# Kernel optimization log

Hardware: AMD Instinct MI355X
Metric: run time of the kernel (lower is better)

Reference implementation:

```python
import jax, jax.numpy as jnp
import numpy as np

N = 10000       # nodes
E = 320000      # edges
D = 256         # feature dim (out_channels)
L = 5           # num_layers


def setup_inputs() -> dict:
    key = jax.random.key(0)
    ks = jax.random.split(key, 8)
    x = jax.random.normal(ks[0], (N, D), dtype=jnp.float32)
    edge_index = jax.random.randint(ks[1], (2, E), 0, N, dtype=jnp.int64)
    edge_attr = jax.random.uniform(ks[2], (E,), dtype=jnp.float32)
    s = 1.0 / np.sqrt(D)
    # per-layer message transform weights [L, D, D]
    weight = jax.random.uniform(ks[3], (L, D, D), minval=-s, maxval=s, dtype=jnp.float32)
    # GRUCell parameters (torch layout: [3D, D] rows = r, z, n)
    w_ih = jax.random.uniform(ks[4], (3 * D, D), minval=-s, maxval=s, dtype=jnp.float32)
    w_hh = jax.random.uniform(ks[5], (3 * D, D), minval=-s, maxval=s, dtype=jnp.float32)
    b_ih = jax.random.uniform(ks[6], (3 * D,), minval=-s, maxval=s, dtype=jnp.float32)
    b_hh = jax.random.uniform(ks[7], (3 * D,), minval=-s, maxval=s, dtype=jnp.float32)
    return {"x": x, "edge_index": edge_index, "edge_attr": edge_attr,
            "weight": weight, "w_ih": w_ih, "w_hh": w_hh,
            "b_ih": b_ih, "b_hh": b_hh}


def _gru_cell(inp, h, w_ih, w_hh, b_ih, b_hh):
    # torch.nn.GRUCell math
    gi = inp @ w_ih.T + b_ih    # [N, 3D]
    gh = h @ w_hh.T + b_hh      # [N, 3D]
    i_r, i_z, i_n = jnp.split(gi, 3, axis=-1)
    h_r, h_z, h_n = jnp.split(gh, 3, axis=-1)
    r = jax.nn.sigmoid(i_r + h_r)
    z = jax.nn.sigmoid(i_z + h_z)
    n = jnp.tanh(i_n + r * h_n)
    return (1.0 - z) * n + z * h


def reference(x, edge_index, edge_attr, weight, w_ih, w_hh, b_ih, b_hh):
    src, dst = edge_index[0], edge_index[1]
    h = x
    for l in range(L):
        m = h @ weight[l]                                   # [N, D]
        msg = m[src] * edge_attr[:, None]                   # [E, D]
        agg = jax.ops.segment_sum(msg, dst, num_segments=N)  # [N, D]
        h = _gru_cell(agg, h, w_ih, w_hh, b_ih, b_hh)
    return h
```

## Files before the change

### kernel.cpp

```cpp
#include <hip/hip_runtime.h>
#include <hip/hip_bf16.h>

#define NN 10000
#define NPAD 10048
#define EE 320000
#define DD 256
#define LL 5

typedef __bf16 bf16x8 __attribute__((ext_vector_type(8)));
typedef __bf16 bf16x4 __attribute__((ext_vector_type(4)));
typedef float f32x4 __attribute__((ext_vector_type(4)));

__device__ __forceinline__ void gload_lds16(const void* g, void* l) {
    __builtin_amdgcn_global_load_lds(
        (const __attribute__((address_space(1))) void*)g,
        (__attribute__((address_space(3))) void*)l, 16, 0, 0);
}


__global__ void zero_deg_k(int* __restrict__ deg) {
    int i = blockIdx.x * blockDim.x + threadIdx.x;
    if (i < NN) deg[i] = 0;
}

__global__ void hist_k(const int* __restrict__ dst, int* __restrict__ deg) {
    int e = blockIdx.x * blockDim.x + threadIdx.x;
    if (e < EE) atomicAdd(&deg[dst[e]], 1);
}

__global__ void scan_k(const int* __restrict__ deg, int* __restrict__ row_start,
                       int* __restrict__ cursor) {
    __shared__ int sums[1024];
    const int CH = 10;
    int t = threadIdx.x;
    int base = t * CH;
    int loc[CH];
    int s = 0;
#pragma unroll
    for (int i = 0; i < CH; i++) {
        int v = (base + i < NN) ? deg[base + i] : 0;
        loc[i] = s;
        s += v;
    }
    sums[t] = s;
    __syncthreads();
    for (int off = 1; off < 1024; off <<= 1) {
        int v = (t >= off) ? sums[t - off] : 0;
        __syncthreads();
        sums[t] += v;
        __syncthreads();
    }
    int pre = (t == 0) ? 0 : sums[t - 1];
#pragma unroll
    for (int i = 0; i < CH; i++) {
        int idx = base + i;
        if (idx < NN) {
            int v = pre + loc[i];
            row_start[idx] = v;
            cursor[idx] = v;
        }
    }
    if (t == 1023) row_start[NN] = sums[1023];
}

__global__ void fill_k(const int* __restrict__ ei, const float* __restrict__ attr,
                       int* __restrict__ cursor, int* __restrict__ ssrc,
                       float* __restrict__ sattr) {
    int e = blockIdx.x * blockDim.x + threadIdx.x;
    if (e < EE) {
        int dv = ei[EE + e];
        int p = atomicAdd(&cursor[dv], 1);
        ssrc[p] = ei[e];
        sattr[p] = attr[e];
    }
}


__global__ void transpose_wb_k(const float* __restrict__ W, __bf16* __restrict__ Wt) {
    __shared__ float t[32][33];
    int l = blockIdx.z;
    int bx = blockIdx.x * 32;
    int by = blockIdx.y * 32;
    for (int i = threadIdx.y; i < 32; i += 8)
        t[i][threadIdx.x] = W[l * 65536 + (by + i) * DD + bx + threadIdx.x];
    __syncthreads();
    for (int i = threadIdx.y; i < 32; i += 8)
        Wt[l * 65536 + (bx + i) * DD + by + threadIdx.x] = (__bf16)t[threadIdx.x][i];
}

__global__ void conv_gruw_k(const float* __restrict__ w_ih, const float* __restrict__ w_hh,
                            __bf16* __restrict__ wihb, __bf16* __restrict__ whhb) {
    int i = blockIdx.x * blockDim.x + threadIdx.x;
    if (i < 768 * 256) {
        wihb[i] = (__bf16)w_ih[i];
        whhb[i] = (__bf16)w_hh[i];
    }
}

__global__ void conv_x_k(const float* __restrict__ x, float* __restrict__ hb,
                         __bf16* __restrict__ hbf) {
    int i = blockIdx.x * blockDim.x + threadIdx.x;
    if (i < NN * DD) {
        float v = x[i];
        hb[i] = v;
        hbf[i] = (__bf16)v;
    }
}

__global__ void pad_zero_k(__bf16* __restrict__ a, __bf16* __restrict__ b,
                           __bf16* __restrict__ c, __bf16* __restrict__ d) {
    int i = blockIdx.x * blockDim.x + threadIdx.x;
    if (i < (NPAD - NN) * DD) {
        a[NN * DD + i] = (__bf16)0.f;
        b[NN * DD + i] = (__bf16)0.f;
        c[NN * DD + i] = (__bf16)0.f;
        d[NN * DD + i] = (__bf16)0.f;
    }
}


__global__ __launch_bounds__(256, 2)
void gemm_m_k(const __bf16* __restrict__ hbf, const __bf16* __restrict__ wt,
              __bf16* __restrict__ mout) {
    __shared__ __bf16 sA[64][32];
    __shared__ __bf16 sB[64][32];
    int tid = threadIdx.x;
    int wave = tid >> 6, lane = tid & 63;
    int ln = lane & 15, quad = lane >> 4;
    int rowBlock = blockIdx.x * 64;
    int colBlock = blockIdx.y * 64;
    int rowHalf = (wave >> 1) * 32;
    int colHalf = (wave & 1) * 32;
    int r4 = lane >> 2;
    int kb = (lane & 3) * 8;

    f32x4 acc[2][2] = {};

    for (int k0 = 0; k0 < DD; k0 += 32) {
        __syncthreads();
#pragma unroll
        for (int ii = 0; ii < 2; ii++) {
            int rg = (wave & 1) * 2 + ii;
            const __bf16* src;
            __bf16* dst;
            if (wave < 2) {
                src = hbf + (size_t)(rowBlock + rg * 16 + r4) * DD + k0 + kb;
                dst = &sA[rg * 16][0];
            } else {
                src = wt + (size_t)(colBlock + rg * 16 + r4) * DD + k0 + kb;
                dst = &sB[rg * 16][0];
            }
            gload_lds16(src, dst);
        }
        __syncthreads();

        bf16x8 af[2], bf[2];
#pragma unroll
        for (int i = 0; i < 2; i++)
            af[i] = *(const bf16x8*)&sA[rowHalf + i * 16 + ln][quad * 8];
#pragma unroll
        for (int cc = 0; cc < 2; cc++)
            bf[cc] = *(const bf16x8*)&sB[colHalf + cc * 16 + ln][quad * 8];
#pragma unroll
        for (int nf = 0; nf < 2; nf++)
#pragma unroll
            for (int cc = 0; cc < 2; cc++)
                acc[nf][cc] = __builtin_amdgcn_mfma_f32_16x16x32_bf16(af[nf], bf[cc], acc[nf][cc], 0, 0, 0);
    }
#pragma unroll
    for (int nf = 0; nf < 2; nf++)
#pragma unroll
        for (int r = 0; r < 4; r++) {
            int n = rowBlock + rowHalf + nf * 16 + quad * 4 + r;
#pragma unroll
            for (int cc = 0; cc < 2; cc++) {
                int d = colBlock + colHalf + cc * 16 + ln;
                mout[(size_t)n * DD + d] = (__bf16)acc[nf][cc][r];
            }
        }
}


__global__ __launch_bounds__(256)
void aggregate_bf_k(const __bf16* __restrict__ m, const int* __restrict__ row_start,
                    const int* __restrict__ ssrc, const float* __restrict__ sattr,
                    __bf16* __restrict__ aggb) {
    __shared__ int sIdx[4][64];
    __shared__ float sAtt[4][64];
    int w = threadIdx.x >> 6, lane = threadIdx.x & 63;
    int n = blockIdx.x * 4 + w;
    int s0 = row_start[n], s1 = row_start[n + 1];
    int half = lane >> 5;
    int c8 = (lane & 31) * 8;

    float acc[8] = {0.f, 0.f, 0.f, 0.f, 0.f, 0.f, 0.f, 0.f};

    for (int base = s0; base < s1; base += 64) {
        int cnt = min(64, s1 - base);
        if (lane < cnt) {
            sIdx[w][lane] = ssrc[base + lane];
            sAtt[w][lane] = sattr[base + lane];
        }
        int t = 0;
        for (; t + 8 <= cnt; t += 8) {
#pragma unroll
            for (int u = 0; u < 4; u++) {
                int e = t + u * 2 + half;
                int s = sIdx[w][e];
                float ww = sAtt[w][e];
                bf16x8 v = *(const bf16x8*)(m + (size_t)s * DD + c8);
#pragma unroll
                for (int i = 0; i < 8; i++) acc[i] += (float)v[i] * ww;
            }
        }
        for (; t + 2 <= cnt; t += 2) {
            int e = t + half;
            int s = sIdx[w][e];
            float ww = sAtt[w][e];
            bf16x8 v = *(const bf16x8*)(m + (size_t)s * DD + c8);
#pragma unroll
            for (int i = 0; i < 8; i++) acc[i] += (float)v[i] * ww;
        }
        if (t < cnt && half == 0) {
            int s = sIdx[w][t];
            float ww = sAtt[w][t];
            bf16x8 v = *(const bf16x8*)(m + (size_t)s * DD + c8);
#pragma unroll
            for (int i = 0; i < 8; i++) acc[i] += (float)v[i] * ww;
        }
    }

#pragma unroll
    for (int i = 0; i < 8; i++) acc[i] += __shfl_xor(acc[i], 32, 64);

    if (half == 0) {
        bf16x8 o;
#pragma unroll
        for (int i = 0; i < 8; i++) o[i] = (__bf16)acc[i];
        *(bf16x8*)(aggb + (size_t)n * DD + c8) = o;
    }
}


__global__ __launch_bounds__(256, 2)
void gru_mfma_k(const __bf16* __restrict__ aggb, const __bf16* __restrict__ hbf,
                const float* __restrict__ hin,
                const __bf16* __restrict__ wih, const __bf16* __restrict__ whh,
                const float* __restrict__ b_ih, const float* __restrict__ b_hh,
                float* __restrict__ hout, __bf16* __restrict__ hbfout) {
    __shared__ __bf16 sA[2][64][32];
    __shared__ __bf16 sB[6][64][32];
    int tid = threadIdx.x;
    int wave = tid >> 6, lane = tid & 63;
    int ln = lane & 15, quad = lane >> 4;
    int nodeBlock = blockIdx.x * 64;
    int colBlock = blockIdx.y * 64;
    int nodeHalf = (wave >> 1) * 32;
    int colHalf = (wave & 1) * 32;
    int r4 = lane >> 2;
    int kb = (lane & 3) * 8;

    f32x4 acc[6][2][2] = {};

    for (int k0 = 0; k0 < DD; k0 += 32) {
        __syncthreads();
#pragma unroll
        for (int ii = 0; ii < 8; ii++) {
            int idx = wave * 8 + ii;
            const __bf16* src;
            __bf16* dst;
            if (idx < 8) {
                int s = idx >> 2;
                int rg = idx & 3;
                const __bf16* A = s ? hbf : aggb;
                src = A + (size_t)(nodeBlock + rg * 16 + r4) * DD + k0 + kb;
                dst = &sA[s][rg * 16][0];
            } else {
                int j = idx - 8;
                int g6 = j >> 2;
                int rg = j & 3;
                const __bf16* B = (g6 < 3) ? wih : whh;
                int brow = (g6 % 3) * 256 + colBlock + rg * 16 + r4;
                src = B + (size_t)brow * DD + k0 + kb;
                dst = &sB[g6][rg * 16][0];
            }
            gload_lds16(src, dst);
        }
        __syncthreads();

        bf16x8 aA[2], aH[2];
#pragma unroll
        for (int nf = 0; nf < 2; nf++) {
            aA[nf] = *(const bf16x8*)&sA[0][nodeHalf + nf * 16 + ln][quad * 8];
            aH[nf] = *(const bf16x8*)&sA[1][nodeHalf + nf * 16 + ln][quad * 8];
        }
#pragma unroll
        for (int g = 0; g < 3; g++) {
#pragma unroll
            for (int cc = 0; cc < 2; cc++) {
                bf16x8 bI = *(const bf16x8*)&sB[g][colHalf + cc * 16 + ln][quad * 8];
                bf16x8 bH = *(const bf16x8*)&sB[3 + g][colHalf + cc * 16 + ln][quad * 8];
#pragma unroll
                for (int nf = 0; nf < 2; nf++) {
                    acc[g][nf][cc] = __builtin_amdgcn_mfma_f32_16x16x32_bf16(aA[nf], bI, acc[g][nf][cc], 0, 0, 0);
                    acc[3 + g][nf][cc] = __builtin_amdgcn_mfma_f32_16x16x32_bf16(aH[nf], bH, acc[3 + g][nf][cc], 0, 0, 0);
                }
            }
        }
    }

#pragma unroll
    for (int nf = 0; nf < 2; nf++) {
#pragma unroll
        for (int r = 0; r < 4; r++) {
            int n = nodeBlock + nodeHalf + nf * 16 + quad * 4 + r;
            if (n >= NN) continue;
#pragma unroll
            for (int cc = 0; cc < 2; cc++) {
                int d = colBlock + colHalf + cc * 16 + ln;
                float ir = acc[0][nf][cc][r] + b_ih[d];
                float iz = acc[1][nf][cc][r] + b_ih[d + 256];
                float in_ = acc[2][nf][cc][r] + b_ih[d + 512];
                float hr = acc[3][nf][cc][r] + b_hh[d];
                float hz = acc[4][nf][cc][r] + b_hh[d + 256];
                float hn = acc[5][nf][cc][r] + b_hh[d + 512];
                float rr = 1.f / (1.f + __expf(-(ir + hr)));
                float zz = 1.f / (1.f + __expf(-(iz + hz)));
                float ax = in_ + rr * hn;
                float e2 = __expf(-2.f * ax);
                float nnv = 2.f / (1.f + e2) - 1.f;
                float hp = hin[(size_t)n * DD + d];
                float o = (1.f - zz) * nnv + zz * hp;
                hout[(size_t)n * DD + d] = o;
                hbfout[(size_t)n * DD + d] = (__bf16)o;
            }
        }
    }
}


extern "C" void kernel_launch(void* const* d_in, const int* in_sizes, int n_in,
                              void* d_out, int out_size, void* d_ws, size_t ws_size,
                              hipStream_t stream) {
    const float* x = (const float*)d_in[0];
    const int* edge_index = (const int*)d_in[1];
    const float* edge_attr = (const float*)d_in[2];
    const float* weight = (const float*)d_in[3];
    const float* w_ih = (const float*)d_in[4];
    const float* w_hh = (const float*)d_in[5];
    const float* b_ih = (const float*)d_in[6];
    const float* b_hh = (const float*)d_in[7];

    size_t off = 0;
    char* base = (char*)d_ws;
    auto carve = [&](size_t bytes) -> void* {
        void* p = base + off;
        off += (bytes + 255) & ~(size_t)255;
        return p;
    };
    float* hb = (float*)carve((size_t)NPAD * DD * 4);
    __bf16* hbfA = (__bf16*)carve((size_t)NPAD * DD * 2);
    __bf16* hbfB = (__bf16*)carve((size_t)NPAD * DD * 2);
    __bf16* mb = (__bf16*)carve((size_t)NPAD * DD * 2);
    __bf16* aggb = (__bf16*)carve((size_t)NPAD * DD * 2);
    __bf16* wtb = (__bf16*)carve((size_t)LL * DD * DD * 2);
    __bf16* wihb = (__bf16*)carve((size_t)768 * DD * 2);
    __bf16* whhb = (__bf16*)carve((size_t)768 * DD * 2);
    int* deg = (int*)carve((size_t)NN * 4);
    int* row_start = (int*)carve((size_t)(NN + 1) * 4);
    int* cursor = (int*)carve((size_t)NN * 4);
    int* ssrc = (int*)carve((size_t)EE * 4);
    float* sattr = (float*)carve((size_t)EE * 4);
    (void)ws_size;

    transpose_wb_k<<<dim3(8, 8, LL), dim3(32, 8), 0, stream>>>(weight, wtb);
    conv_gruw_k<<<(768 * 256 + 255) / 256, 256, 0, stream>>>(w_ih, w_hh, wihb, whhb);
    conv_x_k<<<(NN * DD + 255) / 256, 256, 0, stream>>>(x, hb, hbfA);
    pad_zero_k<<<((NPAD - NN) * DD + 255) / 256, 256, 0, stream>>>(hbfA, hbfB, mb, aggb);

    zero_deg_k<<<(NN + 255) / 256, 256, 0, stream>>>(deg);
    hist_k<<<(EE + 255) / 256, 256, 0, stream>>>(edge_index + EE, deg);
    scan_k<<<1, 1024, 0, stream>>>(deg, row_start, cursor);
    fill_k<<<(EE + 255) / 256, 256, 0, stream>>>(edge_index, edge_attr, cursor, ssrc, sattr);

    float* hA = hb;
    float* hB = (float*)d_out;
    __bf16* hbfIn = hbfA;
    __bf16* hbfOut = hbfB;
    for (int l = 0; l < LL; l++) {
        gemm_m_k<<<dim3(157, 4), 256, 0, stream>>>(hbfIn, wtb + (size_t)l * DD * DD, mb);
        aggregate_bf_k<<<2500, 256, 0, stream>>>(mb, row_start, ssrc, sattr, aggb);
        gru_mfma_k<<<dim3(157, 4), 256, 0, stream>>>(aggb, hbfIn, hA, wihb, whhb,
                                                     b_ih, b_hh, hB, hbfOut);
        float* t = hA; hA = hB; hB = t;
        __bf16* tb = hbfIn; hbfIn = hbfOut; hbfOut = tb;
    }
}
```

Measured before the change: 385.5 us.

## Fuse per-layer GEMM, aggregate and GRU into persistent kernel with grid barriers

Replaces the 15 per-layer launches with one persistent kernel of 256 blocks that loops over layers. Blocks stride over GEMM tiles, aggregation groups and GRU tiles, with a software global barrier between phases. The GRU tile is narrowed to 32 columns so there are more tiles to share across blocks, and the prep kernels are merged into one. This removes launch overhead and inter-kernel gaps, but adds spin-barrier cost, leaves only 256 blocks, and relies on every block being resident at once.

```diff
diff --git a/kernel.cpp b/kernel.cpp
--- a/kernel.cpp
+++ b/kernel.cpp
@@ -6,9 +6,9 @@
 #define EE 320000
 #define DD 256
 #define LL 5
+#define NBLK 256
 
 typedef __bf16 bf16x8 __attribute__((ext_vector_type(8)));
-typedef __bf16 bf16x4 __attribute__((ext_vector_type(4)));
 typedef float f32x4 __attribute__((ext_vector_type(4)));
 
 __device__ __forceinline__ void gload_lds16(const void* g, void* l) {
@@ -18,61 +18,22 @@
 }
 
 
-__global__ void zero_deg_k(int* __restrict__ deg) {
-    int i = blockIdx.x * blockDim.x + threadIdx.x;
-    if (i < NN) deg[i] = 0;
-}
-
-__global__ void hist_k(const int* __restrict__ dst, int* __restrict__ deg) {
-    int e = blockIdx.x * blockDim.x + threadIdx.x;
-    if (e < EE) atomicAdd(&deg[dst[e]], 1);
-}
-
-__global__ void scan_k(const int* __restrict__ deg, int* __restrict__ row_start,
-                       int* __restrict__ cursor) {
-    __shared__ int sums[1024];
-    const int CH = 10;
-    int t = threadIdx.x;
-    int base = t * CH;
-    int loc[CH];
-    int s = 0;
-#pragma unroll
-    for (int i = 0; i < CH; i++) {
-        int v = (base + i < NN) ? deg[base + i] : 0;
-        loc[i] = s;
-        s += v;
-    }
-    sums[t] = s;
+__device__ __forceinline__ void gbar(int* bar, int nb) {
     __syncthreads();
-    for (int off = 1; off < 1024; off <<= 1) {
-        int v = (t >= off) ? sums[t - off] : 0;
-        __syncthreads();
-        sums[t] += v;
-        __syncthreads();
-    }
-    int pre = (t == 0) ? 0 : sums[t - 1];
-#pragma unroll
-    for (int i = 0; i < CH; i++) {
-        int idx = base + i;
-        if (idx < NN) {
-            int v = pre + loc[i];
-            row_start[idx] = v;
-            cursor[idx] = v;
-        }
-    }
-    if (t == 1023) row_start[NN] = sums[1023];
-}
-
-__global__ void fill_k(const int* __restrict__ ei, const float* __restrict__ attr,
-                       int* __restrict__ cursor, int* __restrict__ ssrc,
-                       float* __restrict__ sattr) {
-    int e = blockIdx.x * blockDim.x + threadIdx.x;
-    if (e < EE) {
-        int dv = ei[EE + e];
-        int p = atomicAdd(&cursor[dv], 1);
-        ssrc[p] = ei[e];
-        sattr[p] = attr[e];
-    }
+    if (threadIdx.x == 0) {
+        __threadfence();
+        int g = __hip_atomic_load(bar + 1, __ATOMIC_RELAXED, __HIP_MEMORY_SCOPE_AGENT);
+        int a = __hip_atomic_fetch_add(bar, 1, __ATOMIC_ACQ_REL, __HIP_MEMORY_SCOPE_AGENT);
+        if (a == nb - 1) {
+            __hip_atomic_store(bar, 0, __ATOMIC_RELAXED, __HIP_MEMORY_SCOPE_AGENT);
+            __hip_atomic_fetch_add(bar + 1, 1, __ATOMIC_RELEASE, __HIP_MEMORY_SCOPE_AGENT);
+        } else {
+            while (__hip_atomic_load(bar + 1, __ATOMIC_ACQUIRE, __HIP_MEMORY_SCOPE_AGENT) == g)
+                __builtin_amdgcn_s_sleep(1);
+        }
+        __threadfence();
+    }
+    __syncthreads();
 }
 
 
@@ -88,47 +49,89 @@
         Wt[l * 65536 + (bx + i) * DD + by + threadIdx.x] = (__bf16)t[threadIdx.x][i];
 }
 
-__global__ void conv_gruw_k(const float* __restrict__ w_ih, const float* __restrict__ w_hh,
-                            __bf16* __restrict__ wihb, __bf16* __restrict__ whhb) {
+__global__ void prep_k(const float* __restrict__ w_ih, const float* __restrict__ w_hh,
+                       const float* __restrict__ x,
+                       __bf16* __restrict__ wihb, __bf16* __restrict__ whhb,
+                       float* __restrict__ hb, __bf16* __restrict__ hbfA,
+                       __bf16* __restrict__ hbfB, __bf16* __restrict__ mb,
+                       __bf16* __restrict__ aggb, int* __restrict__ deg,
+                       int* __restrict__ bar) {
     int i = blockIdx.x * blockDim.x + threadIdx.x;
-    if (i < 768 * 256) {
-        wihb[i] = (__bf16)w_ih[i];
-        whhb[i] = (__bf16)w_hh[i];
-    }
-}
-
-__global__ void conv_x_k(const float* __restrict__ x, float* __restrict__ hb,
-                         __bf16* __restrict__ hbf) {
-    int i = blockIdx.x * blockDim.x + threadIdx.x;
-    if (i < NN * DD) {
-        float v = x[i];
-        hb[i] = v;
-        hbf[i] = (__bf16)v;
-    }
-}
-
-__global__ void pad_zero_k(__bf16* __restrict__ a, __bf16* __restrict__ b,
-                           __bf16* __restrict__ c, __bf16* __restrict__ d) {
-    int i = blockIdx.x * blockDim.x + threadIdx.x;
+    if (i < NN * DD) { float v = x[i]; hb[i] = v; hbfA[i] = (__bf16)v; }
+    if (i < 768 * 256) { wihb[i] = (__bf16)w_ih[i]; whhb[i] = (__bf16)w_hh[i]; }
     if (i < (NPAD - NN) * DD) {
-        a[NN * DD + i] = (__bf16)0.f;
-        b[NN * DD + i] = (__bf16)0.f;
-        c[NN * DD + i] = (__bf16)0.f;
-        d[NN * DD + i] = (__bf16)0.f;
-    }
-}
-
-
-__global__ __launch_bounds__(256, 2)
-void gemm_m_k(const __bf16* __restrict__ hbf, const __bf16* __restrict__ wt,
-              __bf16* __restrict__ mout) {
-    __shared__ __bf16 sA[64][32];
-    __shared__ __bf16 sB[64][32];
+        hbfA[NN * DD + i] = (__bf16)0.f;
+        hbfB[NN * DD + i] = (__bf16)0.f;
+        mb[NN * DD + i] = (__bf16)0.f;
+        aggb[NN * DD + i] = (__bf16)0.f;
+    }
+    if (i < NN) deg[i] = 0;
+    if (i < 2) bar[i] = 0;
+}
+
+__global__ void hist_k(const int* __restrict__ dst, int* __restrict__ deg) {
+    int e = blockIdx.x * blockDim.x + threadIdx.x;
+    if (e < EE) atomicAdd(&deg[dst[e]], 1);
+}
+
+__global__ void scan_k(const int* __restrict__ deg, int* __restrict__ row_start,
+                       int* __restrict__ cursor) {
+    __shared__ int sums[1024];
+    const int CH = 10;
+    int t = threadIdx.x;
+    int base = t * CH;
+    int loc[CH];
+    int s = 0;
+#pragma unroll
+    for (int i = 0; i < CH; i++) {
+        int v = (base + i < NN) ? deg[base + i] : 0;
+        loc[i] = s;
+        s += v;
+    }
+    sums[t] = s;
+    __syncthreads();
+    for (int off = 1; off < 1024; off <<= 1) {
+        int v = (t >= off) ? sums[t - off] : 0;
+        __syncthreads();
+        sums[t] += v;
+        __syncthreads();
+    }
+    int pre = (t == 0) ? 0 : sums[t - 1];
+#pragma unroll
+    for (int i = 0; i < CH; i++) {
+        int idx = base + i;
+        if (idx < NN) {
+            int v = pre + loc[i];
+            row_start[idx] = v;
+            cursor[idx] = v;
+        }
+    }
+    if (t == 1023) row_start[NN] = sums[1023];
+}
+
+__global__ void fill_k(const int* __restrict__ ei, const float* __restrict__ attr,
+                       int* __restrict__ cursor, int* __restrict__ ssrc,
+                       float* __restrict__ sattr) {
+    int e = blockIdx.x * blockDim.x + threadIdx.x;
+    if (e < EE) {
+        int dv = ei[EE + e];
+        int p = atomicAdd(&cursor[dv], 1);
+        ssrc[p] = ei[e];
+        sattr[p] = attr[e];
+    }
+}
+
+
+__device__ __forceinline__ void gemm_tile(int t, const __bf16* __restrict__ hbf,
+                                          const __bf16* __restrict__ wt,
+                                          __bf16* __restrict__ mout, char* smraw) {
+    __bf16* sA = (__bf16*)smraw;
+    __bf16* sB = (__bf16*)(smraw + 4096);
     int tid = threadIdx.x;
     int wave = tid >> 6, lane = tid & 63;
     int ln = lane & 15, quad = lane >> 4;
-    int rowBlock = blockIdx.x * 64;
-    int colBlock = blockIdx.y * 64;
+    int rowBlock = (t >> 2) * 64;
+    int colBlock = (t & 3) * 64;
     int rowHalf = (wave >> 1) * 32;
     int colHalf = (wave & 1) * 32;
     int r4 = lane >> 2;
@@ -145,10 +148,10 @@
             __bf16* dst;
             if (wave < 2) {
                 src = hbf + (size_t)(rowBlock + rg * 16 + r4) * DD + k0 + kb;
-                dst = &sA[rg * 16][0];
+                dst = sA + rg * 512;
             } else {
                 src = wt + (size_t)(colBlock + rg * 16 + r4) * DD + k0 + kb;
-                dst = &sB[rg * 16][0];
+                dst = sB + rg * 512;
             }
             gload_lds16(src, dst);
         }
@@ -157,10 +160,10 @@
         bf16x8 af[2], bf[2];
 #pragma unroll
         for (int i = 0; i < 2; i++)
-            af[i] = *(const bf16x8*)&sA[rowHalf + i * 16 + ln][quad * 8];
+            af[i] = *(const bf16x8*)(sA + (rowHalf + i * 16 + ln) * 32 + quad * 8);
 #pragma unroll
         for (int cc = 0; cc < 2; cc++)
-            bf[cc] = *(const bf16x8*)&sB[colHalf + cc * 16 + ln][quad * 8];
+            bf[cc] = *(const bf16x8*)(sB + (colHalf + cc * 16 + ln) * 32 + quad * 8);
 #pragma unroll
         for (int nf = 0; nf < 2; nf++)
 #pragma unroll
@@ -180,15 +183,15 @@
         }
 }
 
-
-__global__ __launch_bounds__(256)
-void aggregate_bf_k(const __bf16* __restrict__ m, const int* __restrict__ row_start,
-                    const int* __restrict__ ssrc, const float* __restrict__ sattr,
-                    __bf16* __restrict__ aggb) {
-    __shared__ int sIdx[4][64];
-    __shared__ float sAtt[4][64];
+__device__ __forceinline__ void agg_group(int g, const __bf16* __restrict__ m,
+                                          const int* __restrict__ row_start,
+                                          const int* __restrict__ ssrc,
+                                          const float* __restrict__ sattr,
+                                          __bf16* __restrict__ aggb, char* smraw) {
+    int* sIdx = (int*)smraw;
+    float* sAtt = (float*)(smraw + 1024);
     int w = threadIdx.x >> 6, lane = threadIdx.x & 63;
-    int n = blockIdx.x * 4 + w;
+    int n = g * 4 + w;
     int s0 = row_start[n], s1 = row_start[n + 1];
     int half = lane >> 5;
     int c8 = (lane & 31) * 8;
@@ -198,16 +201,16 @@
     for (int base = s0; base < s1; base += 64) {
         int cnt = min(64, s1 - base);
         if (lane < cnt) {
-            sIdx[w][lane] = ssrc[base + lane];
-            sAtt[w][lane] = sattr[base + lane];
+            sIdx[w * 64 + lane] = ssrc[base + lane];
+            sAtt[w * 64 + lane] = sattr[base + lane];
         }
         int t = 0;
         for (; t + 8 <= cnt; t += 8) {
 #pragma unroll
             for (int u = 0; u < 4; u++) {
                 int e = t + u * 2 + half;
-                int s = sIdx[w][e];
-                float ww = sAtt[w][e];
+                int s = sIdx[w * 64 + e];
+                float ww = sAtt[w * 64 + e];
                 bf16x8 v = *(const bf16x8*)(m + (size_t)s * DD + c8);
 #pragma unroll
                 for (int i = 0; i < 8; i++) acc[i] += (float)v[i] * ww;
@@ -215,15 +218,15 @@
         }
         for (; t + 2 <= cnt; t += 2) {
             int e = t + half;
-            int s = sIdx[w][e];
-            float ww = sAtt[w][e];
+            int s = sIdx[w * 64 + e];
+            float ww = sAtt[w * 64 + e];
             bf16x8 v = *(const bf16x8*)(m + (size_t)s * DD + c8);
 #pragma unroll
             for (int i = 0; i < 8; i++) acc[i] += (float)v[i] * ww;
         }
         if (t < cnt && half == 0) {
-            int s = sIdx[w][t];
-            float ww = sAtt[w][t];
+            int s = sIdx[w * 64 + t];
+            float ww = sAtt[w * 64 + t];
             bf16x8 v = *(const bf16x8*)(m + (size_t)s * DD + c8);
 #pragma unroll
             for (int i = 0; i < 8; i++) acc[i] += (float)v[i] * ww;
@@ -241,32 +244,34 @@
     }
 }
 
-
-__global__ __launch_bounds__(256, 2)
-void gru_mfma_k(const __bf16* __restrict__ aggb, const __bf16* __restrict__ hbf,
-                const float* __restrict__ hin,
-                const __bf16* __restrict__ wih, const __bf16* __restrict__ whh,
-                const float* __restrict__ b_ih, const float* __restrict__ b_hh,
-                float* __restrict__ hout, __bf16* __restrict__ hbfout) {
-    __shared__ __bf16 sA[2][64][32];
-    __shared__ __bf16 sB[6][64][32];
+__device__ __forceinline__ void gru_tile(int t, const __bf16* __restrict__ aggb,
+                                         const __bf16* __restrict__ hbf,
+                                         const float* __restrict__ hin,
+                                         const __bf16* __restrict__ wih,
+                                         const __bf16* __restrict__ whh,
+                                         const float* __restrict__ b_ih,
+                                         const float* __restrict__ b_hh,
+                                         float* __restrict__ hout,
+                                         __bf16* __restrict__ hbfout, char* smraw) {
+    __bf16* sA = (__bf16*)smraw;
+    __bf16* sB = (__bf16*)(smraw + 8192);
     int tid = threadIdx.x;
     int wave = tid >> 6, lane = tid & 63;
     int ln = lane & 15, quad = lane >> 4;
-    int nodeBlock = blockIdx.x * 64;
-    int colBlock = blockIdx.y * 64;
+    int nodeBlock = (t >> 3) * 64;
+    int colBlock = (t & 7) * 32;
     int nodeHalf = (wave >> 1) * 32;
-    int colHalf = (wave & 1) * 32;
+    int colHalf = (wave & 1) * 16;
     int r4 = lane >> 2;
     int kb = (lane & 3) * 8;
 
-    f32x4 acc[6][2][2] = {};
+    f32x4 acc[6][2] = {};
 
     for (int k0 = 0; k0 < DD; k0 += 32) {
         __syncthreads();
 #pragma unroll
-        for (int ii = 0; ii < 8; ii++) {
-            int idx = wave * 8 + ii;
+        for (int ii = 0; ii < 5; ii++) {
+            int idx = wave * 5 + ii;
             const __bf16* src;
             __bf16* dst;
             if (idx < 8) {
@@ -274,15 +279,15 @@
                 int rg = idx & 3;
                 const __bf16* A = s ? hbf : aggb;
                 src = A + (size_t)(nodeBlock + rg * 16 + r4) * DD + k0 + kb;
-                dst = &sA[s][rg * 16][0];
+                dst = sA + s * 2048 + rg * 512;
             } else {
                 int j = idx - 8;
-                int g6 = j >> 2;
-                int rg = j & 3;
+                int g6 = j >> 1;
+                int rg = j & 1;
                 const __bf16* B = (g6 < 3) ? wih : whh;
                 int brow = (g6 % 3) * 256 + colBlock + rg * 16 + r4;
                 src = B + (size_t)brow * DD + k0 + kb;
-                dst = &sB[g6][rg * 16][0];
+                dst = sB + g6 * 1024 + rg * 512;
             }
             gload_lds16(src, dst);
         }
@@ -291,20 +296,17 @@
         bf16x8 aA[2], aH[2];
 #pragma unroll
         for (int nf = 0; nf < 2; nf++) {
-            aA[nf] = *(const bf16x8*)&sA[0][nodeHalf + nf * 16 + ln][quad * 8];
-            aH[nf] = *(const bf16x8*)&sA[1][nodeHalf + nf * 16 + ln][quad * 8];
+            aA[nf] = *(const bf16x8*)(sA + (nodeHalf + nf * 16 + ln) * 32 + quad * 8);
+            aH[nf] = *(const bf16x8*)(sA + 2048 + (nodeHalf + nf * 16 + ln) * 32 + quad * 8);
         }
 #pragma unroll
         for (int g = 0; g < 3; g++) {
-#pragma unroll
-            for (int cc = 0; cc < 2; cc++) {
-                bf16x8 bI = *(const bf16x8*)&sB[g][colHalf + cc * 16 + ln][quad * 8];
-                bf16x8 bH = *(const bf16x8*)&sB[3 + g][colHalf + cc * 16 + ln][quad * 8];
-#pragma unroll
-                for (int nf = 0; nf < 2; nf++) {
-                    acc[g][nf][cc] = __builtin_amdgcn_mfma_f32_16x16x32_bf16(aA[nf], bI, acc[g][nf][cc], 0, 0, 0);
-                    acc[3 + g][nf][cc] = __builtin_amdgcn_mfma_f32_16x16x32_bf16(aH[nf], bH, acc[3 + g][nf][cc], 0, 0, 0);
-                }
+            bf16x8 bI = *(const bf16x8*)(sB + g * 1024 + (colHalf + ln) * 32 + quad * 8);
+            bf16x8 bH = *(const bf16x8*)(sB + (3 + g) * 1024 + (colHalf + ln) * 32 + quad * 8);
+#pragma unroll
+            for (int nf = 0; nf < 2; nf++) {
+                acc[g][nf] = __builtin_amdgcn_mfma_f32_16x16x32_bf16(aA[nf], bI, acc[g][nf], 0, 0, 0);
+                acc[3 + g][nf] = __builtin_amdgcn_mfma_f32_16x16x32_bf16(aH[nf], bH, acc[3 + g][nf], 0, 0, 0);
             }
         }
     }
@@ -315,26 +317,57 @@
         for (int r = 0; r < 4; r++) {
             int n = nodeBlock + nodeHalf + nf * 16 + quad * 4 + r;
             if (n >= NN) continue;
-#pragma unroll
-            for (int cc = 0; cc < 2; cc++) {
-                int d = colBlock + colHalf + cc * 16 + ln;
-                float ir = acc[0][nf][cc][r] + b_ih[d];
-                float iz = acc[1][nf][cc][r] + b_ih[d + 256];
-                float in_ = acc[2][nf][cc][r] + b_ih[d + 512];
-                float hr = acc[3][nf][cc][r] + b_hh[d];
-                float hz = acc[4][nf][cc][r] + b_hh[d + 256];
-                float hn = acc[5][nf][cc][r] + b_hh[d + 512];
-                float rr = 1.f / (1.f + __expf(-(ir + hr)));
-                float zz = 1.f / (1.f + __expf(-(iz + hz)));
-                float ax = in_ + rr * hn;
-                float e2 = __expf(-2.f * ax);
-                float nnv = 2.f / (1.f + e2) - 1.f;
-                float hp = hin[(size_t)n * DD + d];
-                float o = (1.f - zz) * nnv + zz * hp;
-                hout[(size_t)n * DD + d] = o;
-                hbfout[(size_t)n * DD + d] = (__bf16)o;
-            }
-        }
+            int d = colBlock + colHalf + ln;
+            float ir = acc[0][nf][r] + b_ih[d];
+            float iz = acc[1][nf][r] + b_ih[d + 256];
+            float in_ = acc[2][nf][r] + b_ih[d + 512];
+            float hr = acc[3][nf][r] + b_hh[d];
+            float hz = acc[4][nf][r] + b_hh[d + 256];
+            float hn = acc[5][nf][r] + b_hh[d + 512];
+            float rr = 1.f / (1.f + __expf(-(ir + hr)));
+            float zz = 1.f / (1.f + __expf(-(iz + hz)));
+            float ax = in_ + rr * hn;
+            float e2 = __expf(-2.f * ax);
+            float nnv = 2.f / (1.f + e2) - 1.f;
+            float hp = hin[(size_t)n * DD + d];
+            float o = (1.f - zz) * nnv + zz * hp;
+            hout[(size_t)n * DD + d] = o;
+            hbfout[(size_t)n * DD + d] = (__bf16)o;
+        }
+    }
+}
+
+
+__global__ __launch_bounds__(256, 2)
+void ggnn_mega_k(const __bf16* __restrict__ wtb, const __bf16* __restrict__ wihb,
+                 const __bf16* __restrict__ whhb, const float* __restrict__ b_ih,
+                 const float* __restrict__ b_hh, const int* __restrict__ row_start,
+                 const int* __restrict__ ssrc, const float* __restrict__ sattr,
+                 float* __restrict__ hb, float* __restrict__ outp,
+                 __bf16* __restrict__ hbfA, __bf16* __restrict__ hbfB,
+                 __bf16* __restrict__ mb, __bf16* __restrict__ aggb,
+                 int* __restrict__ bar) {
+    __shared__ __align__(16) char smraw[20480];
+    int bid = blockIdx.x, nb = gridDim.x;
+
+    for (int l = 0; l < LL; l++) {
+        const __bf16* hbfIn = (l & 1) ? hbfB : hbfA;
+        __bf16* hbfOut = (l & 1) ? hbfA : hbfB;
+        const float* hIn = (l & 1) ? outp : hb;
+        float* hOut = (l & 1) ? hb : outp;
+        const __bf16* wt = wtb + (size_t)l * DD * DD;
+
+        for (int t = bid; t < 628; t += nb)
+            gemm_tile(t, hbfIn, wt, mb, smraw);
+        gbar(bar, nb);
+
+        for (int g = bid; g < 2500; g += nb)
+            agg_group(g, mb, row_start, ssrc, sattr, aggb, smraw);
+        gbar(bar, nb);
+
+        for (int t = bid; t < 1256; t += nb)
+            gru_tile(t, aggb, hbfIn, hIn, wihb, whhb, b_ih, b_hh, hOut, hbfOut, smraw);
+        if (l != LL - 1) gbar(bar, nb);
     }
 }
 
@@ -371,28 +404,17 @@
     int* cursor = (int*)carve((size_t)NN * 4);
     int* ssrc = (int*)carve((size_t)EE * 4);
     float* sattr = (float*)carve((size_t)EE * 4);
+    int* bar = (int*)carve(256);
     (void)ws_size;
 
     transpose_wb_k<<<dim3(8, 8, LL), dim3(32, 8), 0, stream>>>(weight, wtb);
-    conv_gruw_k<<<(768 * 256 + 255) / 256, 256, 0, stream>>>(w_ih, w_hh, wihb, whhb);
-    conv_x_k<<<(NN * DD + 255) / 256, 256, 0, stream>>>(x, hb, hbfA);
-    pad_zero_k<<<((NPAD - NN) * DD + 255) / 256, 256, 0, stream>>>(hbfA, hbfB, mb, aggb);
-
-    zero_deg_k<<<(NN + 255) / 256, 256, 0, stream>>>(deg);
+    prep_k<<<(NN * DD + 255) / 256, 256, 0, stream>>>(w_ih, w_hh, x, wihb, whhb,
+                                                      hb, hbfA, hbfB, mb, aggb, deg, bar);
     hist_k<<<(EE + 255) / 256, 256, 0, stream>>>(edge_index + EE, deg);
     scan_k<<<1, 1024, 0, stream>>>(deg, row_start, cursor);
     fill_k<<<(EE + 255) / 256, 256, 0, stream>>>(edge_index, edge_attr, cursor, ssrc, sattr);
 
-    float* hA = hb;
-    float* hB = (float*)d_out;
-    __bf16* hbfIn = hbfA;
-    __bf16* hbfOut = hbfB;
-    for (int l = 0; l < LL; l++) {
-        gemm_m_k<<<dim3(157, 4), 256, 0, stream>>>(hbfIn, wtb + (size_t)l * DD * DD, mb);
-        aggregate_bf_k<<<2500, 256, 0, stream>>>(mb, row_start, ssrc, sattr, aggb);
-        gru_mfma_k<<<dim3(157, 4), 256, 0, stream>>>(aggb, hbfIn, hA, wihb, whhb,
-                                                     b_ih, b_hh, hB, hbfOut);
-        float* t = hA; hA = hB; hB = t;
-        __bf16* tb = hbfIn; hbfIn = hbfOut; hbfOut = tb;
-    }
-}
+    ggnn_mega_k<<<NBLK, 256, 0, stream>>>(wtb, wihb, whhb, b_ih, b_hh,
+                                          row_start, ssrc, sattr,
+                                          hb, (float*)d_out, hbfA, hbfB, mb, aggb, bar);
+}
```

After: 1.234 ms. 220% more time.
